# Kernel tuning notes

Measured on AMD Instinct MI355X. Metric: run time of the kernel, lower is better.

Reference implementation:

```python
import jax, jax.numpy as jnp
import numpy as np

N = 50000          # nodes
E = 800000         # edges (before self loops)
IC = 16            # in_channels; pos = x[:, :3]
H = (64, 64, 128, 128)
OUT = 8
INS = (IC, IC + H[0], IC + H[0] + H[1], IC + H[0] + H[1] + H[2])


def _lin_w(k, fi, fo):
    s = 1.0 / np.sqrt(fi)
    return jax.random.uniform(k, (fi, fo), minval=-s, maxval=s, dtype=jnp.float32)


def setup_inputs() -> dict:
    key = jax.random.key(0)
    ks = jax.random.split(key, 64)
    inp = {
        "x": jax.random.normal(ks[0], (N, IC), dtype=jnp.float32),
        "edge_index": jax.random.randint(ks[1], (2, E), 0, N, dtype=jnp.int32),
    }
    ki = 2
    for i, (fi, fo) in enumerate(zip(INS, H), start=1):
        inp[f"Wl{i}"] = _lin_w(ks[ki], fi, fo); ki += 1   # lin (values), no bias
        inp[f"Ws{i}"] = _lin_w(ks[ki], fi, fo); ki += 1   # lin_src, no bias
        inp[f"Wd{i}"] = _lin_w(ks[ki], fi, fo); ki += 1   # lin_dst, no bias
        inp[f"Wp{i}"] = _lin_w(ks[ki], 3, fo); ki += 1    # pos_nn = Linear(3, fo)
        inp[f"bp{i}"] = jnp.zeros((fo,), jnp.float32)
    inp["Wm1"] = _lin_w(ks[ki], IC + sum(H), 64); ki += 1
    inp["bm1"] = jnp.zeros((64,), jnp.float32)
    inp["Wm2"] = _lin_w(ks[ki], 64, OUT); ki += 1
    inp["bm2"] = jnp.zeros((OUT,), jnp.float32)
    return inp


def _pt_conv(h, pos, src, dst, Wl, Ws, Wd, Wp, bp, n):
    """PointTransformerConv: per-channel softmax attention over incoming edges."""
    a_src = h @ Ws                               # alpha_j part  [N, F]
    a_dst = h @ Wd                               # alpha_i part  [N, F]
    v = h @ Wl                                   # values        [N, F]
    delta = (pos[dst] - pos[src]) @ Wp + bp      # pos_nn(pos_i - pos_j)  [E, F]
    alpha = a_dst[dst] - a_src[src] + delta      # [E, F]
    m = jax.ops.segment_max(alpha, dst, num_segments=n)
    ea = jnp.exp(alpha - m[dst])
    s = jax.ops.segment_sum(ea, dst, num_segments=n)
    attn = ea / s[dst]                           # segment softmax (self loops -> s > 0)
    return jax.ops.segment_sum(attn * (v[src] + delta), dst, num_segments=n)


def reference(x, edge_index, Wl1, Ws1, Wd1, Wp1, bp1, Wl2, Ws2, Wd2, Wp2, bp2,
              Wl3, Ws3, Wd3, Wp3, bp3, Wl4, Ws4, Wd4, Wp4, bp4, Wm1, bm1, Wm2, bm2):
    n = x.shape[0]
    pos = x[:, :3]
    loop = jnp.arange(n, dtype=edge_index.dtype)
    src = jnp.concatenate([edge_index[0], loop])  # PyG add_self_loops (default True)
    dst = jnp.concatenate([edge_index[1], loop])
    lrelu = lambda v: jax.nn.leaky_relu(v, 0.01)
    x1 = lrelu(_pt_conv(x, pos, src, dst, Wl1, Ws1, Wd1, Wp1, bp1, n))
    h2 = jnp.concatenate([x, x1], 1)
    x2 = lrelu(_pt_conv(h2, pos, src, dst, Wl2, Ws2, Wd2, Wp2, bp2, n))
    h3 = jnp.concatenate([x, x1, x2], 1)
    x3 = lrelu(_pt_conv(h3, pos, src, dst, Wl3, Ws3, Wd3, Wp3, bp3, n))
    h4 = jnp.concatenate([x, x1, x2, x3], 1)
    x4 = lrelu(_pt_conv(h4, pos, src, dst, Wl4, Ws4, Wd4, Wp4, bp4, n))
    out = jnp.concatenate([x, x1, x2, x3, x4], 1)  # dropout = identity (eval mode)
    out = out @ Wm1 + bm1
    return out @ Wm2 + bm2
```

## Files before the change

kernel.cpp:

```cpp
#include <hip/hip_runtime.h>
#include <hip/hip_bf16.h>
#include <hip/hip_fp16.h>
#include <math.h>

#define N_NODES 50000
#define N_EDGES 800000
#define ET (N_EDGES + N_NODES)
#define HTOT 400
#define SENTINEL 50000u

#define SCAN_CHUNK 1024
#define NSCB ((N_NODES + SCAN_CHUNK - 1) / SCAN_CHUNK)

typedef __attribute__((ext_vector_type(4))) float f32x4;
typedef __attribute__((ext_vector_type(8))) short bf16x8;

static const int INS_h[4] = {16, 80, 144, 272};
static const int K32_h[4] = {32, 96, 160, 288};
static const int HO_h[4]  = {64, 64, 128, 128};

#define LOG2E_F 1.4426950408889634f


struct PrepArgs {
    const float* x; __hip_bfloat16* h; int* deg;
    const float* Ws0; const float* Wl0;
    const float* Ws1; const float* Wl1;
    const float* Ws2; const float* Wl2;
    const float* Ws3; const float* Wl3;
    const float* Wm1;
    __hip_bfloat16* Wt0; __hip_bfloat16* Wt1; __hip_bfloat16* Wt2;
    __hip_bfloat16* Wt3; __hip_bfloat16* WtF;
    ushort* av;
    const float* Wp0; const float* bp0;
    const float* Wp1; const float* bp1;
    const float* Wp2; const float* bp2;
    const float* Wp3; const float* bp3;
    uint* wph0; uint* wph1; uint* wph2; uint* wph3;
};

__device__ inline void concat1(const float* __restrict__ W0, const float* __restrict__ W1,
                               int K, int K32, int fo, __hip_bfloat16* __restrict__ Wt, int i) {
    int c = i / K32, kk = i - c * K32;
    float v = 0.f;
    if (kk < K) v = (c < fo) ? W0[kk * fo + c] : W1[kk * fo + (c - fo)];
    Wt[i] = __float2bfloat16(v);
}

#define PREP_TOTAL 1008848

__global__ __launch_bounds__(256) void prep_kernel(PrepArgs a) {
    int i = blockIdx.x * 256 + threadIdx.x;
    if (i < 800000) {
        int n = i >> 4, c = i & 15;
        a.h[n * HTOT + c] = __float2bfloat16(a.x[i]);
        return;
    }
    i -= 800000;
    if (i < 50000) { a.deg[i] = 0; return; }
    i -= 50000;
    if (i < 4096)  { concat1(a.Ws0, a.Wl0, 16, 32, 64, a.Wt0, i); return; }
    i -= 4096;
    if (i < 12288) { concat1(a.Ws1, a.Wl1, 80, 96, 64, a.Wt1, i); return; }
    i -= 12288;
    if (i < 40960) { concat1(a.Ws2, a.Wl2, 144, 160, 128, a.Wt2, i); return; }
    i -= 40960;
    if (i < 73728) { concat1(a.Ws3, a.Wl3, 272, 288, 128, a.Wt3, i); return; }
    i -= 73728;
    if (i < 26624) {
        int c = i / 416, kk = i - c * 416;
        float v = (kk < 400) ? a.Wm1[kk * 64 + c] : 0.f;
        a.WtF[i] = __float2bfloat16(v);
        return;
    }
    i -= 26624;
    if (i < 384) {
        if (i < 128) a.av[50000 * 128 + i] = (i < 64)  ? 0xFC00 : 0;
        else { int j = i - 128; a.av[50000 * 256 + j] = (j < 128) ? 0xFC00 : 0; }
        return;
    }
    i -= 384;
    if (i < 768) {
        const float* Wp; const float* bpp; uint* dst; int fo; int q = i;
        if (q < 128)      { Wp = a.Wp0; bpp = a.bp0; dst = a.wph0; fo = 64; }
        else if (q < 256) { q -= 128; Wp = a.Wp1; bpp = a.bp1; dst = a.wph1; fo = 64; }
        else if (q < 512) { q -= 256; Wp = a.Wp2; bpp = a.bp2; dst = a.wph2; fo = 128; }
        else              { q -= 512; Wp = a.Wp3; bpp = a.bp3; dst = a.wph3; fo = 128; }
        int hf = fo >> 1;
        int arr = q / hf, pr = q - arr * hf;
        int c = 2 * pr;
        float v0, v1;
        if (arr < 3) { v0 = Wp[arr * fo + c]; v1 = Wp[arr * fo + c + 1]; }
        else         { v0 = bpp[c]; v1 = bpp[c + 1]; }
        __half2 hh = __floats2half2_rn(v0, v1);
        dst[q] = *reinterpret_cast<uint*>(&hh);
    }
}


__global__ void hist_kernel(const int* __restrict__ ei, int* __restrict__ deg) {
    int e = blockIdx.x * blockDim.x + threadIdx.x;
    if (e >= ET) return;
    int dst = (e < N_EDGES) ? ei[N_EDGES + e] : (e - N_EDGES);
    atomicAdd(&deg[dst], 1);
}

__global__ __launch_bounds__(256) void scan_p1(const int* __restrict__ deg,
                                               int* __restrict__ bsum) {
    __shared__ int red[256];
    const int b = blockIdx.x, t = threadIdx.x;
    const int base = b * SCAN_CHUNK + t * 4;
    int s = 0;
#pragma unroll
    for (int j = 0; j < 4; ++j) {
        int i = base + j;
        if (i < N_NODES) s += deg[i];
    }
    red[t] = s;
    __syncthreads();
    for (int off = 128; off > 0; off >>= 1) {
        if (t < off) red[t] += red[t + off];
        __syncthreads();
    }
    if (t == 0) bsum[b] = red[0];
}

__global__ __launch_bounds__(256) void scan_p3(const int* __restrict__ deg,
                                               const int* __restrict__ bsum,
                                               int* __restrict__ row_ptr,
                                               int* __restrict__ cursor) {
    __shared__ int ts[256];
    __shared__ int sb[2];
    const int b = blockIdx.x, t = threadIdx.x;
    if (t < 64) {
        int v = (t < NSCB) ? bsum[t] : 0;
        int inc = v;
#pragma unroll
        for (int off = 1; off < 64; off <<= 1) {
            int u = __shfl_up(inc, off);
            if (t >= off) inc += u;
        }
        if (t == b) sb[0] = inc - v;
        if (t == 63) sb[1] = inc;
    }
    const int base = b * SCAN_CHUNK + t * 4;
    int v[4];
    int s = 0;
#pragma unroll
    for (int j = 0; j < 4; ++j) {
        int i = base + j;
        v[j] = (i < N_NODES) ? deg[i] : 0;
        s += v[j];
    }
    ts[t] = s;
    __syncthreads();
    for (int off = 1; off < 256; off <<= 1) {
        int u = (t >= off) ? ts[t - off] : 0;
        __syncthreads();
        ts[t] += u;
        __syncthreads();
    }
    int excl = sb[0] + ts[t] - s;
#pragma unroll
    for (int j = 0; j < 4; ++j) {
        int i = base + j;
        if (i < N_NODES) {
            row_ptr[i] = excl;
            cursor[i] = excl;
            excl += v[j];
        }
    }
    if (b == 0 && t == 0) row_ptr[N_NODES] = sb[1];
}

__global__ void scatter_kernel(const int* __restrict__ ei, const float* __restrict__ x,
                               int* __restrict__ cursor, uint2* __restrict__ edata) {
    int e = blockIdx.x * blockDim.x + threadIdx.x;
    if (e >= ET) return;
    int src, dst;
    if (e < N_EDGES) { src = ei[e]; dst = ei[N_EDGES + e]; }
    else             { src = dst = e - N_EDGES; }
    int p = atomicAdd(&cursor[dst], 1);
    float4 pd = *(const float4*)&x[dst * 16];
    float4 ps = *(const float4*)&x[src * 16];
    __half dxh = __float2half(pd.x - ps.x);
    __half dyh = __float2half(pd.y - ps.y);
    __half dzh = __float2half(pd.z - ps.z);
    uint w0 = (uint)src | ((uint)__half_as_ushort(dzh) << 16);
    __half2 xy;
    xy.x = dxh; xy.y = dyh;
    edata[p] = make_uint2(w0, *(uint*)&xy);
}


template <bool FUSE>
__global__ __launch_bounds__(256) void gemm3_kernel(
    const __hip_bfloat16* __restrict__ A, int lda,
    const __hip_bfloat16* __restrict__ Wt, int K32,
    const float* __restrict__ bias,
    __half* __restrict__ av, int fo,
    int M, int K, int GXP,
    const float* __restrict__ W2, const float* __restrict__ b2,
    float* __restrict__ out) {
    __shared__ float smemf[9728];
    ushort* sA = (ushort*)smemf;
    ushort* sB = (ushort*)smemf + 10240;
    const int t = threadIdx.x;
    const int bid = blockIdx.x;
    const int gxp = bid % GXP;
    const int gy = bid / GXP;
    const int r0 = gxp * 128, c0 = gy * 64;
    const int w = t >> 6, lane = t & 63;
    const int l15 = lane & 15, l4 = lane >> 4;

    f32x4 acc[2][4];
#pragma unroll
    for (int i = 0; i < 2; ++i)
#pragma unroll
        for (int j = 0; j < 4; ++j) acc[i][j] = (f32x4){0.f, 0.f, 0.f, 0.f};

    const int sr = t >> 2, sq = (t & 3) * 8;
    const int ar1 = min(r0 + sr, M - 1), ar2 = min(r0 + sr + 64, M - 1);
    const size_t a1b = (size_t)ar1 * lda, a2b = (size_t)ar2 * lda;
    const size_t wb = (size_t)(c0 + sr) * K32;
    const int nk = K32 >> 5;

    uint4 ga0, ga1, gb;
    const uint4 z4 = {0u, 0u, 0u, 0u};
    {
        const int kk = sq;
        const bool ok = kk < K;
        ga0 = ok ? *(const uint4*)(A + a1b + kk) : z4;
        ga1 = ok ? *(const uint4*)(A + a2b + kk) : z4;
        gb  = *(const uint4*)(Wt + wb + kk);
        *(uint4*)(sA + sr * 40 + sq) = ga0;
        *(uint4*)(sA + (sr + 64) * 40 + sq) = ga1;
        *(uint4*)(sB + sr * 40 + sq) = gb;
    }
    __syncthreads();

    int buf = 0;
    for (int kc = 0; kc < nk; ++kc) {
        const bool nx = (kc + 1) < nk;
        if (nx) {
            const int kk = (kc + 1) * 32 + sq;
            const bool ok = kk < K;
            ga0 = ok ? *(const uint4*)(A + a1b + kk) : z4;
            ga1 = ok ? *(const uint4*)(A + a2b + kk) : z4;
            gb  = *(const uint4*)(Wt + wb + kk);
        }
        const ushort* bA = sA + buf * 5120 + w * 1280;
        const ushort* bB = sB + buf * 2560;
        bf16x8 af[2], bfr[4];
#pragma unroll
        for (int i = 0; i < 2; ++i)
            af[i] = *(const bf16x8*)(bA + (i * 16 + l15) * 40 + l4 * 8);
#pragma unroll
        for (int j = 0; j < 4; ++j)
            bfr[j] = *(const bf16x8*)(bB + (j * 16 + l15) * 40 + l4 * 8);
#pragma unroll
        for (int i = 0; i < 2; ++i)
#pragma unroll
            for (int j = 0; j < 4; ++j)
                acc[i][j] = __builtin_amdgcn_mfma_f32_16x16x32_bf16(af[i], bfr[j], acc[i][j], 0, 0, 0);
        if (nx) {
            const int ob = buf ^ 1;
            *(uint4*)(sA + ob * 5120 + sr * 40 + sq) = ga0;
            *(uint4*)(sA + ob * 5120 + (sr + 64) * 40 + sq) = ga1;
            *(uint4*)(sB + ob * 2560 + sr * 40 + sq) = gb;
        }
        __syncthreads();
        buf ^= 1;
    }

    if (!FUSE) {
        const int n2 = 2 * fo;
#pragma unroll
        for (int i = 0; i < 2; ++i)
#pragma unroll
            for (int j = 0; j < 4; ++j)
#pragma unroll
                for (int p = 0; p < 4; ++p) {
                    int row = r0 + w * 32 + i * 16 + l4 * 4 + p;
                    int col = c0 + j * 16 + l15;
                    if (row < M) {
                        float vv = acc[i][j][p];
                        if (col < fo) vv *= -LOG2E_F;
                        av[(size_t)row * n2 + col] = __float2half(vv);
                    }
                }
    } else {
#pragma unroll
        for (int i = 0; i < 2; ++i)
#pragma unroll
            for (int j = 0; j < 4; ++j)
#pragma unroll
                for (int p = 0; p < 4; ++p) {
                    int lrow = w * 32 + i * 16 + l4 * 4 + p;
                    int col = j * 16 + l15;
                    smemf[lrow * 68 + col] = acc[i][j][p] + bias[col];
                }
        smemf[8704 + t] = W2[t];
        smemf[8704 + 256 + t] = W2[256 + t];
        __syncthreads();
        const int row = t >> 1, oc = (t & 1) * 4;
        f32x4 o = *(const f32x4*)&b2[oc];
#pragma unroll 8
        for (int k = 0; k < 64; ++k) {
            float a = smemf[row * 68 + k];
            o += a * *(const f32x4*)&smemf[8704 + k * 8 + oc];
        }
        const int grow = r0 + row;
        if (grow < M) *(f32x4*)&out[(size_t)grow * 8 + oc] = o;
    }
}


__device__ inline __half2 h2e2(__half2 a) {
    __half2 r;
    r.x = hexp2(__low2half(a));
    r.y = hexp2(__high2half(a));
    return r;
}

template <int LPE>
__global__ __launch_bounds__(256) void attn_kernel(
    __hip_bfloat16* __restrict__ h,
    const __half* __restrict__ av,
    const uint* __restrict__ wph,
    const int* __restrict__ rowp, const uint2* __restrict__ edata,
    int colbase) {
    constexpr int FO = 8 * LPE;
    constexpr int SLOTS = 64 / LPE;
    const int wid = (blockIdx.x * (int)blockDim.x + (int)threadIdx.x) >> 6;
    if (wid >= N_NODES) return;
    const int lane = threadIdx.x & 63;
    const int e = lane / LPE, lp = lane % LPE;
    const int cb = lp * 8;

    uint4 w0 = *(const uint4*)(wph + 0 * (FO / 2) + lp * 4);
    uint4 w1 = *(const uint4*)(wph + 1 * (FO / 2) + lp * 4);
    uint4 w2 = *(const uint4*)(wph + 2 * (FO / 2) + lp * 4);
    uint4 wb4 = *(const uint4*)(wph + 3 * (FO / 2) + lp * 4);
    const __half2* wp0h = (const __half2*)&w0;
    const __half2* wp1h = (const __half2*)&w1;
    const __half2* wp2h = (const __half2*)&w2;
    const __half2* bph  = (const __half2*)&wb4;

    __half2 s2[4], n2v[4];
    const __half2 hz = __float2half2_rn(0.f);
#pragma unroll
    for (int j = 0; j < 4; ++j) { s2[j] = hz; n2v[j] = hz; }

    const uint* avu = (const uint*)av;
    const __half2 L2E = __float2half2_rn(LOG2E_F);
    const int beg = rowp[wid], end = rowp[wid + 1], last = end - 1;

    uint2 ed_c, ed_n;
    uint4 a_c, v_c, a_n, v_n;
    auto ld = [&](int b, uint2& ed, uint4& a4, uint4& v4) {
        ed = edata[min(b + e, last)];
        const uint src = (b + e < end) ? (ed.x & 0xFFFFu) : SENTINEL;
        const uint* rb = avu + (size_t)src * FO + (cb >> 1);
        a4 = *(const uint4*)rb;
        v4 = *(const uint4*)(rb + FO / 2);
    };
    auto compute = [&](const uint2& ed, const uint4& a4, const uint4& v4) {
        __half2 dz2 = __half2half2(__ushort_as_half((ushort)(ed.x >> 16)));
        __half2 dxy = *(const __half2*)&ed.y;
        __half2 dx2 = __half2half2(__low2half(dxy));
        __half2 dy2 = __half2half2(__high2half(dxy));
        const uint* ap = (const uint*)&a4;
        const uint* vp = (const uint*)&v4;
#pragma unroll
        for (int jj = 0; jj < 4; ++jj) {
            __half2 d  = __hfma2(dx2, wp0h[jj], __hfma2(dy2, wp1h[jj], __hfma2(dz2, wp2h[jj], bph[jj])));
            __half2 a2 = __hfma2(d, L2E, *(const __half2*)&ap[jj]);
            __half2 vd = __hadd2(*(const __half2*)&vp[jj], d);
            __half2 p2 = h2e2(a2);
            s2[jj] = __hadd2(s2[jj], p2);
            n2v[jj] = __hfma2(p2, vd, n2v[jj]);
        }
    };

    ld(beg, ed_c, a_c, v_c);
    for (int base = beg; base < end; base += SLOTS) {
        ld(base + SLOTS, ed_n, a_n, v_n);
        compute(ed_c, a_c, v_c);
        ed_c = ed_n; a_c = a_n; v_c = v_n;
    }

    float s[8], num[8];
#pragma unroll
    for (int jj = 0; jj < 4; ++jj) {
        s[2 * jj]       = __half2float(__low2half(s2[jj]));
        s[2 * jj + 1]   = __half2float(__high2half(s2[jj]));
        num[2 * jj]     = __half2float(__low2half(n2v[jj]));
        num[2 * jj + 1] = __half2float(__high2half(n2v[jj]));
    }
#pragma unroll
    for (int j = 0; j < 8; ++j) {
#pragma unroll
        for (int off = LPE; off < 64; off <<= 1) {
            s[j] += __shfl_xor(s[j], off);
            num[j] += __shfl_xor(num[j], off);
        }
    }
    if (e == 0) {
        ushort o[8];
#pragma unroll
        for (int j = 0; j < 8; ++j) {
            float xi = num[j] / s[j];
            xi = xi > 0.f ? xi : 0.01f * xi;
            __hip_bfloat16 b = __float2bfloat16(xi);
            o[j] = *(ushort*)&b;
        }
        ushort* dst = (ushort*)&h[(size_t)wid * HTOT + colbase + cb];
        *(uint4*)dst = *(uint4*)o;
    }
}


extern "C" void kernel_launch(void* const* d_in, const int* in_sizes, int n_in,
                              void* d_out, int out_size, void* d_ws, size_t ws_size,
                              hipStream_t stream) {
    const float* x = (const float*)d_in[0];
    const int* ei = (const int*)d_in[1];
    const float *Wl[4], *Ws[4], *Wp[4], *bp[4];
    for (int i = 0; i < 4; ++i) {
        Wl[i] = (const float*)d_in[2 + 5 * i];
        Ws[i] = (const float*)d_in[3 + 5 * i];
        Wp[i] = (const float*)d_in[5 + 5 * i];
        bp[i] = (const float*)d_in[6 + 5 * i];
    }
    const float* Wm1 = (const float*)d_in[22];
    const float* bm1 = (const float*)d_in[23];
    const float* Wm2 = (const float*)d_in[24];
    const float* bm2 = (const float*)d_in[25];
    float* out = (float*)d_out;

    char* ws = (char*)d_ws;
    size_t off = 0;
    auto alloc = [&](size_t bytes) -> void* {
        void* p = ws + off;
        off += (bytes + 255) & ~(size_t)255;
        return p;
    };
    __hip_bfloat16* h = (__hip_bfloat16*)alloc((size_t)N_NODES * HTOT * 2);
    __half* av = (__half*)alloc((size_t)(N_NODES + 1) * 256 * 2);
    __hip_bfloat16* Wt0 = (__hip_bfloat16*)alloc((size_t)4096 * 2);
    __hip_bfloat16* Wt1 = (__hip_bfloat16*)alloc((size_t)12288 * 2);
    __hip_bfloat16* Wt2 = (__hip_bfloat16*)alloc((size_t)40960 * 2);
    __hip_bfloat16* Wt3 = (__hip_bfloat16*)alloc((size_t)73728 * 2);
    __hip_bfloat16* WtF = (__hip_bfloat16*)alloc((size_t)26624 * 2);
    uint* wph0 = (uint*)alloc((size_t)128 * 4);
    uint* wph1 = (uint*)alloc((size_t)128 * 4);
    uint* wph2 = (uint*)alloc((size_t)256 * 4);
    uint* wph3 = (uint*)alloc((size_t)256 * 4);
    int* deg = (int*)alloc((size_t)N_NODES * 4);
    int* rowp = (int*)alloc((size_t)(N_NODES + 1) * 4);
    int* cursor = (int*)alloc((size_t)N_NODES * 4);
    int* bsum = (int*)alloc((size_t)(NSCB + 1) * 4);
    uint2* edata = (uint2*)alloc((size_t)ET * 8);
    (void)ws_size; (void)n_in; (void)in_sizes; (void)out_size;

    PrepArgs pa;
    pa.x = x; pa.h = h; pa.deg = deg;
    pa.Ws0 = Ws[0]; pa.Wl0 = Wl[0];
    pa.Ws1 = Ws[1]; pa.Wl1 = Wl[1];
    pa.Ws2 = Ws[2]; pa.Wl2 = Wl[2];
    pa.Ws3 = Ws[3]; pa.Wl3 = Wl[3];
    pa.Wm1 = Wm1;
    pa.Wt0 = Wt0; pa.Wt1 = Wt1; pa.Wt2 = Wt2; pa.Wt3 = Wt3; pa.WtF = WtF;
    pa.av = (ushort*)av;
    pa.Wp0 = Wp[0]; pa.bp0 = bp[0];
    pa.Wp1 = Wp[1]; pa.bp1 = bp[1];
    pa.Wp2 = Wp[2]; pa.bp2 = bp[2];
    pa.Wp3 = Wp[3]; pa.bp3 = bp[3];
    pa.wph0 = wph0; pa.wph1 = wph1; pa.wph2 = wph2; pa.wph3 = wph3;
    prep_kernel<<<(PREP_TOTAL + 255) / 256, 256, 0, stream>>>(pa);

    hist_kernel<<<(ET + 255) / 256, 256, 0, stream>>>(ei, deg);
    scan_p1<<<NSCB, 256, 0, stream>>>(deg, bsum);
    scan_p3<<<NSCB, 256, 0, stream>>>(deg, bsum, rowp, cursor);
    scatter_kernel<<<(ET + 255) / 256, 256, 0, stream>>>(ei, x, cursor, edata);

    const int M = N_NODES;
    const int GXP = (((M + 127) / 128 + 7) / 8) * 8;
    const int nbn = (N_NODES + 3) / 4;
    __hip_bfloat16* Wts[4] = {Wt0, Wt1, Wt2, Wt3};
    uint* wphs[4] = {wph0, wph1, wph2, wph3};
    for (int L = 0; L < 4; ++L) {
        const int K = INS_h[L], K32 = K32_h[L], fo = HO_h[L], n2 = 2 * fo;
        gemm3_kernel<false><<<GXP * (n2 / 64), 256, 0, stream>>>(
            h, HTOT, Wts[L], K32, nullptr, av, fo, M, K, GXP, nullptr, nullptr, nullptr);
        if (fo == 64)
            attn_kernel<8><<<nbn, 256, 0, stream>>>(h, av, wphs[L], rowp, edata, K);
        else
            attn_kernel<16><<<nbn, 256, 0, stream>>>(h, av, wphs[L], rowp, edata, K);
    }
    gemm3_kernel<true><<<GXP, 256, 0, stream>>>(h, HTOT, WtF, 416, bm1,
                                                nullptr, 0, M, 400, GXP, Wm2, bm2, out);
}
```

Before: 349.8 us.

## Fuse CSR build into one cooperative kernel with grid syncs

Replaces the histogram, two scan passes and scatter kernels with a single cooperative kernel of 1024 blocks that separates the phases with grid.sync, removing three kernel launches and the gaps between them. It also pads the edge array with sentinel entries so the attention kernel can drop its min() clamp on edge loads. The cost is grid-wide barriers and grid-stride loops over a fixed grid size, and the kernel depends on a cooperative launch fitting all 1024 blocks at once.

```diff
diff --git a/kernel.cpp b/kernel.cpp
--- a/kernel.cpp
+++ b/kernel.cpp
@@ -1,7 +1,10 @@
 #include <hip/hip_runtime.h>
 #include <hip/hip_bf16.h>
 #include <hip/hip_fp16.h>
+#include <hip/hip_cooperative_groups.h>
 #include <math.h>
+
+namespace cg = cooperative_groups;
 
 #define N_NODES 50000
 #define N_EDGES 800000
@@ -98,98 +101,104 @@
 }
 
 
-__global__ void hist_kernel(const int* __restrict__ ei, int* __restrict__ deg) {
-    int e = blockIdx.x * blockDim.x + threadIdx.x;
-    if (e >= ET) return;
-    int dst = (e < N_EDGES) ? ei[N_EDGES + e] : (e - N_EDGES);
-    atomicAdd(&deg[dst], 1);
-}
-
-__global__ __launch_bounds__(256) void scan_p1(const int* __restrict__ deg,
-                                               int* __restrict__ bsum) {
-    __shared__ int red[256];
-    const int b = blockIdx.x, t = threadIdx.x;
-    const int base = b * SCAN_CHUNK + t * 4;
-    int s = 0;
-#pragma unroll
-    for (int j = 0; j < 4; ++j) {
-        int i = base + j;
-        if (i < N_NODES) s += deg[i];
-    }
-    red[t] = s;
-    __syncthreads();
-    for (int off = 128; off > 0; off >>= 1) {
-        if (t < off) red[t] += red[t + off];
+__global__ __launch_bounds__(256) void csr_kernel(
+    const int* __restrict__ ei, const float* __restrict__ x,
+    int* __restrict__ deg, int* __restrict__ rowp, int* __restrict__ cursor,
+    uint2* __restrict__ edata, int* __restrict__ bsum) {
+    cg::grid_group grid = cg::this_grid();
+    __shared__ int sh[256];
+    __shared__ int sb[2];
+    const int t = threadIdx.x;
+    const int b = blockIdx.x;
+    const int tid = b * 256 + t;
+    const int NT = gridDim.x * 256;
+
+    for (int e = tid; e < ET; e += NT) {
+        int dst = (e < N_EDGES) ? ei[N_EDGES + e] : (e - N_EDGES);
+        atomicAdd(&deg[dst], 1);
+    }
+    grid.sync();
+
+    if (b < NSCB) {
+        const int base = b * SCAN_CHUNK + t * 4;
+        int s = 0;
+#pragma unroll
+        for (int j = 0; j < 4; ++j) {
+            int i = base + j;
+            if (i < N_NODES) s += deg[i];
+        }
+        sh[t] = s;
         __syncthreads();
-    }
-    if (t == 0) bsum[b] = red[0];
-}
-
-__global__ __launch_bounds__(256) void scan_p3(const int* __restrict__ deg,
-                                               const int* __restrict__ bsum,
-                                               int* __restrict__ row_ptr,
-                                               int* __restrict__ cursor) {
-    __shared__ int ts[256];
-    __shared__ int sb[2];
-    const int b = blockIdx.x, t = threadIdx.x;
-    if (t < 64) {
-        int v = (t < NSCB) ? bsum[t] : 0;
-        int inc = v;
-#pragma unroll
-        for (int off = 1; off < 64; off <<= 1) {
-            int u = __shfl_up(inc, off);
-            if (t >= off) inc += u;
-        }
-        if (t == b) sb[0] = inc - v;
-        if (t == 63) sb[1] = inc;
-    }
-    const int base = b * SCAN_CHUNK + t * 4;
-    int v[4];
-    int s = 0;
-#pragma unroll
-    for (int j = 0; j < 4; ++j) {
-        int i = base + j;
-        v[j] = (i < N_NODES) ? deg[i] : 0;
-        s += v[j];
-    }
-    ts[t] = s;
-    __syncthreads();
-    for (int off = 1; off < 256; off <<= 1) {
-        int u = (t >= off) ? ts[t - off] : 0;
+        for (int off = 128; off > 0; off >>= 1) {
+            if (t < off) sh[t] += sh[t + off];
+            __syncthreads();
+        }
+        if (t == 0) bsum[b] = sh[0];
+    }
+    grid.sync();
+
+    if (b < NSCB) {
+        if (t < 64) {
+            int v = (t < NSCB) ? bsum[t] : 0;
+            int inc = v;
+#pragma unroll
+            for (int off = 1; off < 64; off <<= 1) {
+                int u = __shfl_up(inc, off);
+                if (t >= off) inc += u;
+            }
+            if (t == b) sb[0] = inc - v;
+            if (t == 63) sb[1] = inc;
+        }
+        const int base = b * SCAN_CHUNK + t * 4;
+        int v[4];
+        int s = 0;
+#pragma unroll
+        for (int j = 0; j < 4; ++j) {
+            int i = base + j;
+            v[j] = (i < N_NODES) ? deg[i] : 0;
+            s += v[j];
+        }
+        sh[t] = s;
         __syncthreads();
-        ts[t] += u;
-        __syncthreads();
-    }
-    int excl = sb[0] + ts[t] - s;
-#pragma unroll
-    for (int j = 0; j < 4; ++j) {
-        int i = base + j;
-        if (i < N_NODES) {
-            row_ptr[i] = excl;
-            cursor[i] = excl;
-            excl += v[j];
-        }
-    }
-    if (b == 0 && t == 0) row_ptr[N_NODES] = sb[1];
-}
-
-__global__ void scatter_kernel(const int* __restrict__ ei, const float* __restrict__ x,
-                               int* __restrict__ cursor, uint2* __restrict__ edata) {
-    int e = blockIdx.x * blockDim.x + threadIdx.x;
-    if (e >= ET) return;
-    int src, dst;
-    if (e < N_EDGES) { src = ei[e]; dst = ei[N_EDGES + e]; }
-    else             { src = dst = e - N_EDGES; }
-    int p = atomicAdd(&cursor[dst], 1);
-    float4 pd = *(const float4*)&x[dst * 16];
-    float4 ps = *(const float4*)&x[src * 16];
-    __half dxh = __float2half(pd.x - ps.x);
-    __half dyh = __float2half(pd.y - ps.y);
-    __half dzh = __float2half(pd.z - ps.z);
-    uint w0 = (uint)src | ((uint)__half_as_ushort(dzh) << 16);
-    __half2 xy;
-    xy.x = dxh; xy.y = dyh;
-    edata[p] = make_uint2(w0, *(uint*)&xy);
+        for (int off = 1; off < 256; off <<= 1) {
+            int u = (t >= off) ? sh[t - off] : 0;
+            __syncthreads();
+            sh[t] += u;
+            __syncthreads();
+        }
+        int excl = sb[0] + sh[t] - s;
+#pragma unroll
+        for (int j = 0; j < 4; ++j) {
+            int i = base + j;
+            if (i < N_NODES) {
+                rowp[i] = excl;
+                cursor[i] = excl;
+                excl += v[j];
+            }
+        }
+        if (b == 0 && t == 0) rowp[N_NODES] = sb[1];
+    }
+    grid.sync();
+
+    for (int e = tid; e < ET + 128; e += NT) {
+        if (e < ET) {
+            int src, dst;
+            if (e < N_EDGES) { src = ei[e]; dst = ei[N_EDGES + e]; }
+            else             { src = dst = e - N_EDGES; }
+            int p = atomicAdd(&cursor[dst], 1);
+            float4 pd = *(const float4*)&x[dst * 16];
+            float4 ps = *(const float4*)&x[src * 16];
+            __half dxh = __float2half(pd.x - ps.x);
+            __half dyh = __float2half(pd.y - ps.y);
+            __half dzh = __float2half(pd.z - ps.z);
+            uint w0 = (uint)src | ((uint)__half_as_ushort(dzh) << 16);
+            __half2 xy;
+            xy.x = dxh; xy.y = dyh;
+            edata[p] = make_uint2(w0, *(uint*)&xy);
+        } else {
+            edata[e] = make_uint2(SENTINEL, 0u);
+        }
+    }
 }
 
 
@@ -354,12 +363,12 @@
 
     const uint* avu = (const uint*)av;
     const __half2 L2E = __float2half2_rn(LOG2E_F);
-    const int beg = rowp[wid], end = rowp[wid + 1], last = end - 1;
+    const int beg = rowp[wid], end = rowp[wid + 1];
 
     uint2 ed_c, ed_n;
     uint4 a_c, v_c, a_n, v_n;
     auto ld = [&](int b, uint2& ed, uint4& a4, uint4& v4) {
-        ed = edata[min(b + e, last)];
+        ed = edata[b + e];
         const uint src = (b + e < end) ? (ed.x & 0xFFFFu) : SENTINEL;
         const uint* rb = avu + (size_t)src * FO + (cb >> 1);
         a4 = *(const uint4*)rb;
@@ -461,7 +470,7 @@
     int* rowp = (int*)alloc((size_t)(N_NODES + 1) * 4);
     int* cursor = (int*)alloc((size_t)N_NODES * 4);
     int* bsum = (int*)alloc((size_t)(NSCB + 1) * 4);
-    uint2* edata = (uint2*)alloc((size_t)ET * 8);
+    uint2* edata = (uint2*)alloc((size_t)(ET + 128) * 8);
     (void)ws_size; (void)n_in; (void)in_sizes; (void)out_size;
 
     PrepArgs pa;
@@ -480,10 +489,12 @@
     pa.wph0 = wph0; pa.wph1 = wph1; pa.wph2 = wph2; pa.wph3 = wph3;
     prep_kernel<<<(PREP_TOTAL + 255) / 256, 256, 0, stream>>>(pa);
 
-    hist_kernel<<<(ET + 255) / 256, 256, 0, stream>>>(ei, deg);
-    scan_p1<<<NSCB, 256, 0, stream>>>(deg, bsum);
-    scan_p3<<<NSCB, 256, 0, stream>>>(deg, bsum, rowp, cursor);
-    scatter_kernel<<<(ET + 255) / 256, 256, 0, stream>>>(ei, x, cursor, edata);
+    {
+        void* args[] = {(void*)&ei, (void*)&x, (void*)&deg, (void*)&rowp,
+                        (void*)&cursor, (void*)&edata, (void*)&bsum};
+        hipLaunchCooperativeKernel((const void*)csr_kernel, dim3(1024), dim3(256),
+                                   args, 0, stream);
+    }
 
     const int M = N_NODES;
     const int GXP = (((M + 127) / 128 + 7) / 8) * 8;
```

Result: slower. 635.8 us (+81.8%).
